# Kernel optimization log

Hardware: AMD Instinct MI355X
Metric: run time of the kernel (lower is better)

The kernel has to match this reference:

```python
import jax, jax.numpy as jnp
import numpy as np

# Graph/block sizes: 2-hop sampled minibatch
N0, N1, N2 = 655360, 81920, 8192   # src nodes layer0, dst0/src1, dst1 (seeds)
FAN0, FAN1 = 8, 10
E0, E1 = N1 * FAN0, N2 * FAN1       # 655360, 81920
F_IN, H = 128, 256
BN_EPS = 1e-5
L2_EPS = 1e-12


def setup_inputs() -> dict:
    key = jax.random.key(0)
    ks = jax.random.split(key, 16)
    s = 0.05  # param scale
    inp = {
        "x": jax.random.normal(ks[0], (N0, F_IN), jnp.float32),
        "edge_src0": jax.random.randint(ks[1], (E0,), 0, N0, jnp.int32),
        "edge_dst0": jnp.repeat(jnp.arange(N1, dtype=jnp.int32), FAN0),
        "edge_src1": jax.random.randint(ks[2], (E1,), 0, N1, jnp.int32),
        "edge_dst1": jnp.repeat(jnp.arange(N2, dtype=jnp.int32), FAN1),
        "W_pool0": jax.random.normal(ks[3], (F_IN, F_IN), jnp.float32) * s,
        "b_pool0": jnp.zeros((F_IN,), jnp.float32),
        "W_self0": jax.random.normal(ks[4], (F_IN, H), jnp.float32) * s,
        "W_neigh0": jax.random.normal(ks[5], (F_IN, H), jnp.float32) * s,
        "b0": jnp.zeros((H,), jnp.float32),
        "W_pool1": jax.random.normal(ks[6], (H, H), jnp.float32) * s,
        "b_pool1": jnp.zeros((H,), jnp.float32),
        "W_self1": jax.random.normal(ks[7], (H, H), jnp.float32) * s,
        "W_neigh1": jax.random.normal(ks[8], (H, H), jnp.float32) * s,
        "b1": jnp.zeros((H,), jnp.float32),
        "g_bn0": jnp.ones((H,), jnp.float32),
        "be_bn0": jnp.zeros((H,), jnp.float32),
        "W_h": jax.random.normal(ks[9], (H, H), jnp.float32) * s,
        "b_h": jnp.zeros((H,), jnp.float32),
        "g_bnh": jnp.ones((H,), jnp.float32),
        "be_bnh": jnp.zeros((H,), jnp.float32),
        "W_lat": jax.random.normal(ks[10], (H, H), jnp.float32) * s,
        "b_lat": jnp.zeros((H,), jnp.float32),
        "g_bnl": jnp.ones((H,), jnp.float32),
        "be_bnl": jnp.zeros((H,), jnp.float32),
    }
    return inp


def _sage_pool(h, esrc, edst, n_dst, Wp, bp, Ws, Wn, b):
    # DGL SAGEConv aggregator_type='pool':
    # m = relu(fc_pool(h_src)); pooled[v] = max_{u in N(v)} m[u]
    # out = fc_self(h_dst) + fc_neigh(pooled) + bias
    m = jax.nn.relu(h @ Wp + bp)                                  # [N_src, d]
    pooled = jax.ops.segment_max(m[esrc], edst, num_segments=n_dst)
    return h[:n_dst] @ Ws + pooled @ Wn + b


def _l2norm(h):
    n = jnp.sqrt(jnp.sum(h * h, axis=1, keepdims=True))
    return h / jnp.maximum(n, L2_EPS)


def _bn(h, g, b):
    mu = jnp.mean(h, axis=0)
    var = jnp.var(h, axis=0)
    return (h - mu) * jax.lax.rsqrt(var + BN_EPS) * g + b


def reference(x, edge_src0, edge_dst0, edge_src1, edge_dst1,
              W_pool0, b_pool0, W_self0, W_neigh0, b0,
              W_pool1, b_pool1, W_self1, W_neigh1, b1,
              g_bn0, be_bn0, W_h, b_h, g_bnh, be_bnh,
              W_lat, b_lat, g_bnl, be_bnl):
    # layer 0
    h = _sage_pool(x, edge_src0, edge_dst0, N1, W_pool0, b_pool0, W_self0, W_neigh0, b0)
    h = _l2norm(h)
    h = jax.nn.relu(_bn(h, g_bn0, be_bn0))
    # dropout: eval mode (identity)
    h = jax.nn.relu(_bn(h @ W_h + b_h, g_bnh, be_bnh))   # self.hidden
    # layer 1 (last conv)
    h = _sage_pool(h, edge_src1, edge_dst1, N2, W_pool1, b_pool1, W_self1, W_neigh1, b1)
    h = _l2norm(h)
    # self.latent
    h = _bn(h @ W_lat + b_lat, g_bnl, be_bnl)
    return h
```

## Files before the change

### kernel.cpp

```cpp
#include <hip/hip_runtime.h>

typedef unsigned short u16;
typedef unsigned int u32;
typedef float f32x4 __attribute__((ext_vector_type(4)));
typedef int i32x4 __attribute__((ext_vector_type(4)));
typedef __bf16 bf16x8 __attribute__((ext_vector_type(8)));
typedef short s16x8 __attribute__((ext_vector_type(8)));

#define CN0 655360
#define CN1 81920
#define CN2 8192

#define H0_OFF    0ull
#define T_OFF     41943040ull
#define H2_OFF    83886080ull
#define ZZ_OFF    88080384ull
#define WP0F_OFF  96468992ull
#define WC0F_OFF  96501760ull
#define WHF_OFF   96632832ull
#define WP1F_OFF  96763904ull
#define WC1F_OFF  96894976ull
#define WLATF_OFF 97157120ull
#define STAT_OFF  97288192ull
#define SS_OFF    97294336ull

__device__ inline u16 f2bf(float f) {
  u32 u = __builtin_bit_cast(u32, f);
  return (u16)((u + 0x7fffu + ((u >> 16) & 1u)) >> 16);
}
__device__ inline float bf2f(u16 s) {
  return __builtin_bit_cast(float, (u32)s << 16);
}

template <typename V>
__device__ inline auto mfma_sel(V a, V b, f32x4 c, int)
    -> decltype(__builtin_amdgcn_mfma_f32_16x16x32_bf16(a, b, c, 0, 0, 0)) {
  return __builtin_amdgcn_mfma_f32_16x16x32_bf16(a, b, c, 0, 0, 0);
}
template <typename V>
__device__ inline f32x4 mfma_sel(V a, V b, f32x4 c, long) {
  return __builtin_amdgcn_mfma_f32_16x16x32_bf16(
      __builtin_bit_cast(s16x8, a), __builtin_bit_cast(s16x8, b), c, 0, 0, 0);
}
__device__ inline f32x4 MFMA(i32x4 a, i32x4 b, f32x4 c) {
  return mfma_sel(__builtin_bit_cast(bf16x8, a), __builtin_bit_cast(bf16x8, b), c, 0);
}

__device__ void fragify(const float* W0, const float* W1, int Khalf, int N,
                        u16* dst, int tid, int nthr) {
  int K = W1 ? 2 * Khalf : Khalf;
  int ntile = N >> 4;
  int total = (K >> 5) * ntile * 512;
  for (int i = tid; i < total; i += nthr) {
    int j = i & 7;
    int lane = (i >> 3) & 63;
    int nt = (i >> 9) % ntile;
    int kt = i / (512 * ntile);
    int k = kt * 32 + ((lane >> 4) << 3) + j;
    int n = nt * 16 + (lane & 15);
    float v = (k < Khalf) ? W0[k * N + n] : W1[(k - Khalf) * N + n];
    dst[i] = f2bf(v);
  }
}

__global__ void kprep(const float* Wp0, const float* Ws0, const float* Wn0,
                      const float* Wh, const float* Wp1, const float* Ws1,
                      const float* Wn1, const float* Wlat,
                      u16* wp0f, u16* wc0f, u16* whf, u16* wp1f, u16* wc1f,
                      u16* wlatf) {
  int tid = blockIdx.x * blockDim.x + threadIdx.x;
  int nthr = gridDim.x * blockDim.x;
  fragify(Wp0, nullptr, 128, 128, wp0f, tid, nthr);
  fragify(Ws0, Wn0, 128, 256, wc0f, tid, nthr);
  fragify(Wh, nullptr, 256, 256, whf, tid, nthr);
  fragify(Wp1, nullptr, 256, 256, wp1f, tid, nthr);
  fragify(Ws1, Wn1, 256, 256, wc1f, tid, nthr);
  fragify(Wlat, nullptr, 256, 256, wlatf, tid, nthr);
}

__global__ void kfin(const float* __restrict__ stat, float inv_n,
                     const float* __restrict__ g, const float* __restrict__ be,
                     float* __restrict__ ssout) {
  int c = threadIdx.x;
  float mu = stat[c] * inv_n;
  float var = stat[256 + c] * inv_n - mu * mu;
  float sc = g[c] / sqrtf(var + 1e-5f);
  ssout[c] = sc;
  ssout[256 + c] = be[c] - mu * sc;
}

__global__ __launch_bounds__(256, 2)
void k1_layer0(const float* __restrict__ x, const int* __restrict__ esrc,
               const u16* __restrict__ wp0f, const u16* __restrict__ wc0f,
               const float* __restrict__ bp0, const float* __restrict__ b0v,
               u16* __restrict__ h0, float* __restrict__ stat0) {
  __shared__ __align__(16) char lds[81920];
  float* pooled = (float*)(lds + 65536);
  int tid = threadIdx.x, lane = tid & 63, w = tid >> 6;
  int r15 = lane & 15, g = lane >> 4;
  int d0 = blockIdx.x * 32;

  {
    int r = tid;
    int src = esrc[d0 * 8 + r];
    const float* xr = x + (size_t)src * 128;
    u32 rowb = (u32)r * 256, sw = (u32)((r & 7) << 4);
    for (int c = 0; c < 16; ++c) {
      f32x4 p0 = *(const f32x4*)(xr + c * 8);
      f32x4 p1 = *(const f32x4*)(xr + c * 8 + 4);
      union { i32x4 q; u16 h[8]; } pk;
      #pragma unroll
      for (int j = 0; j < 4; ++j) { pk.h[j] = f2bf(p0[j]); pk.h[4 + j] = f2bf(p1[j]); }
      *(i32x4*)(lds + ((rowb + (u32)c * 16) ^ sw)) = pk.q;
    }
  }
  __syncthreads();

  {
    i32x4 afr[4][4];
    #pragma unroll
    for (int rt = 0; rt < 4; ++rt)
      #pragma unroll
      for (int kt = 0; kt < 4; ++kt) {
        u32 r = (u32)(w * 64 + rt * 16 + r15);
        afr[rt][kt] = *(const i32x4*)(lds + ((r * 256 + (u32)kt * 64 + (u32)g * 16) ^ ((r & 7) << 4)));
      }
    for (int nt = 0; nt < 8; ++nt) {
      f32x4 acc[4] = {};
      #pragma unroll
      for (int kt = 0; kt < 4; ++kt) {
        i32x4 b = *(const i32x4*)(wp0f + (((kt * 8 + nt) * 64 + lane) << 3));
        #pragma unroll
        for (int rt = 0; rt < 4; ++rt) acc[rt] = MFMA(afr[rt][kt], b, acc[rt]);
      }
      float bias = bp0[nt * 16 + r15];
      #pragma unroll
      for (int rt = 0; rt < 4; ++rt) {
        float mx = fmaxf(fmaxf(acc[rt][0], acc[rt][1]), fmaxf(acc[rt][2], acc[rt][3]));
        mx = fmaxf(mx + bias, 0.0f);
        mx = fmaxf(mx, __shfl_xor(mx, 16));
        if ((g & 1) == 0)
          pooled[(w * 8 + rt * 2 + (g >> 1)) * 128 + nt * 16 + r15] = mx;
      }
    }
  }
  __syncthreads();

  float* h0buf = (float*)(lds + 16384);
  {
    int i = tid >> 3, seg = tid & 7;
    int k0 = seg * 32;
    u32 sw = (u32)((i & 7) << 4);
    float vals[32];
    if (seg < 4) {
      const float* xr = x + (size_t)(d0 + i) * 128 + k0;
      #pragma unroll
      for (int c4 = 0; c4 < 8; ++c4) {
        f32x4 t = *(const f32x4*)(xr + c4 * 4);
        vals[c4 * 4 + 0] = t[0]; vals[c4 * 4 + 1] = t[1];
        vals[c4 * 4 + 2] = t[2]; vals[c4 * 4 + 3] = t[3];
      }
    } else {
      const float* pr = pooled + i * 128 + (k0 - 128);
      #pragma unroll
      for (int c4 = 0; c4 < 8; ++c4) {
        f32x4 t = *(const f32x4*)(pr + c4 * 4);
        vals[c4 * 4 + 0] = t[0]; vals[c4 * 4 + 1] = t[1];
        vals[c4 * 4 + 2] = t[2]; vals[c4 * 4 + 3] = t[3];
      }
    }
    #pragma unroll
    for (int cc = 0; cc < 4; ++cc) {
      union { i32x4 q; u16 h[8]; } pk;
      #pragma unroll
      for (int j = 0; j < 8; ++j) pk.h[j] = f2bf(vals[cc * 8 + j]);
      *(i32x4*)(lds + (((u32)i * 512 + (u32)(k0 + cc * 8) * 2) ^ sw)) = pk.q;
    }
  }
  __syncthreads();

  {
    f32x4 acc[4][2] = {};
    for (int kt = 0; kt < 8; ++kt) {
      u32 r0 = (u32)r15, r1 = (u32)(16 + r15);
      i32x4 a0 = *(const i32x4*)(lds + ((r0 * 512 + (u32)kt * 64 + (u32)g * 16) ^ ((r0 & 7) << 4)));
      i32x4 a1 = *(const i32x4*)(lds + ((r1 * 512 + (u32)kt * 64 + (u32)g * 16) ^ ((r1 & 7) << 4)));
      #pragma unroll
      for (int n4 = 0; n4 < 4; ++n4) {
        int nt = w * 4 + n4;
        i32x4 b = *(const i32x4*)(wc0f + (((size_t)(kt * 16 + nt) * 64 + lane) << 3));
        acc[n4][0] = MFMA(a0, b, acc[n4][0]);
        acc[n4][1] = MFMA(a1, b, acc[n4][1]);
      }
    }
    #pragma unroll
    for (int n4 = 0; n4 < 4; ++n4) {
      int col = (w * 4 + n4) * 16 + r15;
      float bv = b0v[col];
      #pragma unroll
      for (int rt = 0; rt < 2; ++rt)
        #pragma unroll
        for (int j = 0; j < 4; ++j)
          h0buf[(rt * 16 + g * 4 + j) * 256 + col] = acc[n4][rt][j] + bv;
    }
  }
  __syncthreads();

  {
    int i = tid >> 3, part = tid & 7;
    float* hr = h0buf + i * 256 + part * 32;
    float v[32]; float ss = 0.0f;
    #pragma unroll
    for (int c = 0; c < 32; ++c) { v[c] = hr[c]; ss += v[c] * v[c]; }
    ss += __shfl_xor(ss, 1); ss += __shfl_xor(ss, 2); ss += __shfl_xor(ss, 4);
    float rn = 1.0f / fmaxf(sqrtf(ss), 1e-12f);
    u16* orow = h0 + (size_t)(d0 + i) * 256 + part * 32;
    #pragma unroll
    for (int cc = 0; cc < 4; ++cc) {
      union { i32x4 q; u16 h[8]; } pk;
      #pragma unroll
      for (int j = 0; j < 8; ++j) {
        float nv = v[cc * 8 + j] * rn;
        hr[cc * 8 + j] = nv;
        pk.h[j] = f2bf(nv);
      }
      *(i32x4*)(orow + cc * 8) = pk.q;
    }
  }
  __syncthreads();

  {
    int c = tid; float s1 = 0.0f, s2 = 0.0f;
    for (int r = 0; r < 32; ++r) { float vv = h0buf[r * 256 + c]; s1 += vv; s2 += vv * vv; }
    atomicAdd(&stat0[c], s1); atomicAdd(&stat0[256 + c], s2);
  }
}

template <bool RELU_OUT, bool STATS, bool H2OUT>
__global__ __launch_bounds__(256, 2)
void gemm64(const u16* __restrict__ Ain, const float* __restrict__ ss,
            const u16* __restrict__ Bf, const float* __restrict__ bias,
            u16* __restrict__ Out, float* __restrict__ stat,
            u16* __restrict__ H2out) {
  __shared__ __align__(16) char lds[67584];
  u16* tb = (u16*)(lds + 32768);
  float* scs = (float*)(lds + 65536);
  int tid = threadIdx.x, lane = tid & 63, w = tid >> 6;
  int r15 = lane & 15, g = lane >> 4;
  int d0 = blockIdx.x * 64;
  scs[tid] = ss[tid];
  scs[256 + tid] = ss[256 + tid];
  __syncthreads();

  {
    int i = tid >> 2, part = tid & 3;
    const u16* ar = Ain + (size_t)(d0 + i) * 256 + part * 64;
    u32 sw = (u32)((i & 7) << 4), rowb = (u32)i * 512;
    for (int cc = 0; cc < 8; ++cc) {
      union { i32x4 q; u16 h[8]; } in, out;
      in.q = *(const i32x4*)(ar + cc * 8);
      #pragma unroll
      for (int j = 0; j < 8; ++j) {
        int k = part * 64 + cc * 8 + j;
        float v = fmaxf(bf2f(in.h[j]) * scs[k] + scs[256 + k], 0.0f);
        out.h[j] = f2bf(v);
      }
      *(i32x4*)(lds + ((rowb + (u32)(part * 64 + cc * 8) * 2) ^ sw)) = out.q;
    }
  }
  __syncthreads();

  f32x4 acc[4][4] = {};
  for (int kt = 0; kt < 8; ++kt) {
    i32x4 a[4];
    #pragma unroll
    for (int rt = 0; rt < 4; ++rt) {
      u32 r = (u32)(rt * 16 + r15);
      a[rt] = *(const i32x4*)(lds + ((r * 512 + (u32)kt * 64 + (u32)g * 16) ^ ((r & 7) << 4)));
    }
    #pragma unroll
    for (int n4 = 0; n4 < 4; ++n4) {
      int nt = w * 4 + n4;
      i32x4 b = *(const i32x4*)(Bf + (((size_t)(kt * 16 + nt) * 64 + lane) << 3));
      #pragma unroll
      for (int rt = 0; rt < 4; ++rt) acc[n4][rt] = MFMA(a[rt], b, acc[n4][rt]);
    }
  }
  #pragma unroll
  for (int n4 = 0; n4 < 4; ++n4) {
    int col = (w * 4 + n4) * 16 + r15;
    float bv = bias[col];
    #pragma unroll
    for (int rt = 0; rt < 4; ++rt)
      #pragma unroll
      for (int j = 0; j < 4; ++j) {
        float v = acc[n4][rt][j] + bv;
        if (RELU_OUT) v = fmaxf(v, 0.0f);
        tb[(rt * 16 + g * 4 + j) * 256 + col] = f2bf(v);
      }
  }
  __syncthreads();

  {
    int i = tid >> 2, part = tid & 3;
    u16* orow = Out + (size_t)(d0 + i) * 256 + part * 64;
    const u16* trow = tb + i * 256 + part * 64;
    #pragma unroll
    for (int cc = 0; cc < 8; ++cc)
      *(i32x4*)(orow + cc * 8) = *(const i32x4*)(trow + cc * 8);
  }
  if (STATS) {
    int c = tid; float s1 = 0.0f, s2 = 0.0f;
    for (int r = 0; r < 64; ++r) { float v = bf2f(tb[r * 256 + c]); s1 += v; s2 += v * v; }
    atomicAdd(&stat[c], s1); atomicAdd(&stat[256 + c], s2);
  }
  if (H2OUT && d0 < CN2) {
    int i = tid >> 2, part = tid & 3;
    u16* orow = H2out + (size_t)(d0 + i) * 256 + part * 64;
    u32 sw = (u32)((i & 7) << 4);
    #pragma unroll
    for (int cc = 0; cc < 8; ++cc)
      *(i32x4*)(orow + cc * 8) =
          *(const i32x4*)(lds + (((u32)i * 512 + (u32)(part * 64 + cc * 8) * 2) ^ sw));
  }
}

__global__ __launch_bounds__(256, 2)
void k6_layer1(const int* __restrict__ esrc1, const u16* __restrict__ m1,
               const u16* __restrict__ h2, const u16* __restrict__ wc1f,
               const u16* __restrict__ wlatf, const float* __restrict__ b1v,
               const float* __restrict__ blat, float* __restrict__ zz,
               float* __restrict__ statl) {
  __shared__ __align__(16) char lds[81920];
  float* zbuf = (float*)(lds + 32768);
  int tid = threadIdx.x, lane = tid & 63, w = tid >> 6;
  int r15 = lane & 15, g = lane >> 4;
  int d0 = blockIdx.x * 32;

  {
    int i = tid >> 3, part = tid & 7;
    u32 sw = (u32)((i & 7) << 4);
    const u16* hrow = h2 + (size_t)(d0 + i) * 256 + part * 32;
    #pragma unroll
    for (int cc = 0; cc < 4; ++cc) {
      i32x4 q = *(const i32x4*)(hrow + cc * 8);
      *(i32x4*)(lds + (((u32)i * 1024 + (u32)(part * 32 + cc * 8) * 2) ^ sw)) = q;
    }
    float mx[32];
    #pragma unroll
    for (int c = 0; c < 32; ++c) mx[c] = -1e30f;
    for (int e = 0; e < 10; ++e) {
      int src = esrc1[(d0 + i) * 10 + e];
      const u16* mrow = m1 + (size_t)src * 256 + part * 32;
      #pragma unroll
      for (int cc = 0; cc < 4; ++cc) {
        union { i32x4 q; u16 h[8]; } pk;
        pk.q = *(const i32x4*)(mrow + cc * 8);
        #pragma unroll
        for (int j = 0; j < 8; ++j) mx[cc * 8 + j] = fmaxf(mx[cc * 8 + j], bf2f(pk.h[j]));
      }
    }
    #pragma unroll
    for (int cc = 0; cc < 4; ++cc) {
      union { i32x4 q; u16 h[8]; } pk;
      #pragma unroll
      for (int j = 0; j < 8; ++j) pk.h[j] = f2bf(mx[cc * 8 + j]);
      *(i32x4*)(lds + (((u32)i * 1024 + (u32)(256 + part * 32 + cc * 8) * 2) ^ sw)) = pk.q;
    }
  }
  __syncthreads();

  {
    f32x4 acc[4][2] = {};
    for (int kt = 0; kt < 16; ++kt) {
      u32 r0 = (u32)r15, r1 = (u32)(16 + r15);
      i32x4 a0 = *(const i32x4*)(lds + ((r0 * 1024 + (u32)kt * 64 + (u32)g * 16) ^ ((r0 & 7) << 4)));
      i32x4 a1 = *(const i32x4*)(lds + ((r1 * 1024 + (u32)kt * 64 + (u32)g * 16) ^ ((r1 & 7) << 4)));
      #pragma unroll
      for (int n4 = 0; n4 < 4; ++n4) {
        int nt = w * 4 + n4;
        i32x4 b = *(const i32x4*)(wc1f + (((size_t)(kt * 16 + nt) * 64 + lane) << 3));
        acc[n4][0] = MFMA(a0, b, acc[n4][0]);
        acc[n4][1] = MFMA(a1, b, acc[n4][1]);
      }
    }
    #pragma unroll
    for (int n4 = 0; n4 < 4; ++n4) {
      int col = (w * 4 + n4) * 16 + r15;
      float bv = b1v[col];
      #pragma unroll
      for (int rt = 0; rt < 2; ++rt)
        #pragma unroll
        for (int j = 0; j < 4; ++j)
          zbuf[(rt * 16 + g * 4 + j) * 256 + col] = acc[n4][rt][j] + bv;
    }
  }
  __syncthreads();

  {
    int i = tid >> 3, part = tid & 7;
    float* zr = zbuf + i * 256 + part * 32;
    float v[32]; float ss = 0.0f;
    #pragma unroll
    for (int c = 0; c < 32; ++c) { v[c] = zr[c]; ss += v[c] * v[c]; }
    ss += __shfl_xor(ss, 1); ss += __shfl_xor(ss, 2); ss += __shfl_xor(ss, 4);
    float rn = 1.0f / fmaxf(sqrtf(ss), 1e-12f);
    u32 sw = (u32)((i & 7) << 4);
    #pragma unroll
    for (int cc = 0; cc < 4; ++cc) {
      union { i32x4 q; u16 h[8]; } pk;
      #pragma unroll
      for (int j = 0; j < 8; ++j) pk.h[j] = f2bf(v[cc * 8 + j] * rn);
      *(i32x4*)(lds + 65536 + (((u32)i * 512 + (u32)(part * 32 + cc * 8) * 2) ^ sw)) = pk.q;
    }
  }
  __syncthreads();

  {
    f32x4 acc[4][2] = {};
    for (int kt = 0; kt < 8; ++kt) {
      u32 r0 = (u32)r15, r1 = (u32)(16 + r15);
      i32x4 a0 = *(const i32x4*)(lds + 65536 + ((r0 * 512 + (u32)kt * 64 + (u32)g * 16) ^ ((r0 & 7) << 4)));
      i32x4 a1 = *(const i32x4*)(lds + 65536 + ((r1 * 512 + (u32)kt * 64 + (u32)g * 16) ^ ((r1 & 7) << 4)));
      #pragma unroll
      for (int n4 = 0; n4 < 4; ++n4) {
        int nt = w * 4 + n4;
        i32x4 b = *(const i32x4*)(wlatf + (((size_t)(kt * 16 + nt) * 64 + lane) << 3));
        acc[n4][0] = MFMA(a0, b, acc[n4][0]);
        acc[n4][1] = MFMA(a1, b, acc[n4][1]);
      }
    }
    #pragma unroll
    for (int n4 = 0; n4 < 4; ++n4) {
      int col = (w * 4 + n4) * 16 + r15;
      float bv = blat[col];
      #pragma unroll
      for (int rt = 0; rt < 2; ++rt)
        #pragma unroll
        for (int j = 0; j < 4; ++j)
          zbuf[(rt * 16 + g * 4 + j) * 256 + col] = acc[n4][rt][j] + bv;
    }
  }
  __syncthreads();

  {
    int i = tid >> 3, part = tid & 7;
    float* zr = zbuf + i * 256 + part * 32;
    float* orow = zz + (size_t)(d0 + i) * 256 + part * 32;
    #pragma unroll
    for (int c = 0; c < 32; c += 4) *(f32x4*)(orow + c) = *(const f32x4*)(zr + c);
  }
  {
    int c = tid; float s1 = 0.0f, s2 = 0.0f;
    for (int r = 0; r < 32; ++r) { float v = zbuf[r * 256 + c]; s1 += v; s2 += v * v; }
    atomicAdd(&statl[c], s1); atomicAdd(&statl[256 + c], s2);
  }
}

__global__ void k7_out(const float* __restrict__ zz, const float* __restrict__ ssl,
                       float* __restrict__ out) {
  int idx = blockIdx.x * 256 + threadIdx.x;
  int e0 = idx * 4;
  int c = e0 & 255;
  f32x4 v = *(const f32x4*)(zz + e0);
  f32x4 sc = *(const f32x4*)(ssl + c);
  f32x4 sh = *(const f32x4*)(ssl + 256 + c);
  *(f32x4*)(out + e0) = v * sc + sh;
}

extern "C" void kernel_launch(void* const* d_in, const int* in_sizes, int n_in,
                              void* d_out, int out_size, void* d_ws, size_t ws_size,
                              hipStream_t stream) {
  const float* x     = (const float*)d_in[0];
  const int*   es0   = (const int*)d_in[1];
  const int*   es1   = (const int*)d_in[3];
  const float* Wp0   = (const float*)d_in[5];
  const float* bp0   = (const float*)d_in[6];
  const float* Ws0   = (const float*)d_in[7];
  const float* Wn0   = (const float*)d_in[8];
  const float* b0v   = (const float*)d_in[9];
  const float* Wp1   = (const float*)d_in[10];
  const float* bp1   = (const float*)d_in[11];
  const float* Ws1   = (const float*)d_in[12];
  const float* Wn1   = (const float*)d_in[13];
  const float* b1v   = (const float*)d_in[14];
  const float* gbn0  = (const float*)d_in[15];
  const float* bebn0 = (const float*)d_in[16];
  const float* Wh    = (const float*)d_in[17];
  const float* bh    = (const float*)d_in[18];
  const float* gbnh  = (const float*)d_in[19];
  const float* bebnh = (const float*)d_in[20];
  const float* Wlat  = (const float*)d_in[21];
  const float* blat  = (const float*)d_in[22];
  const float* gbnl  = (const float*)d_in[23];
  const float* bebnl = (const float*)d_in[24];

  char* ws = (char*)d_ws;
  u16* h0    = (u16*)(ws + H0_OFF);
  u16* tban  = (u16*)(ws + T_OFF);
  u16* m1    = (u16*)(ws + H0_OFF);
  u16* h2    = (u16*)(ws + H2_OFF);
  float* zz  = (float*)(ws + ZZ_OFF);
  u16* wp0f  = (u16*)(ws + WP0F_OFF);
  u16* wc0f  = (u16*)(ws + WC0F_OFF);
  u16* whf   = (u16*)(ws + WHF_OFF);
  u16* wp1f  = (u16*)(ws + WP1F_OFF);
  u16* wc1f  = (u16*)(ws + WC1F_OFF);
  u16* wlatf = (u16*)(ws + WLATF_OFF);
  float* stat = (float*)(ws + STAT_OFF);
  float* ssv  = (float*)(ws + SS_OFF);

  hipMemsetAsync(stat, 0, 6 * 256 * sizeof(float), stream);
  kprep<<<64, 256, 0, stream>>>(Wp0, Ws0, Wn0, Wh, Wp1, Ws1, Wn1, Wlat,
                                wp0f, wc0f, whf, wp1f, wc1f, wlatf);
  k1_layer0<<<CN1 / 32, 256, 0, stream>>>(x, es0, wp0f, wc0f, bp0, b0v, h0, stat);
  kfin<<<1, 256, 0, stream>>>(stat, 1.0f / CN1, gbn0, bebn0, ssv);
  gemm64<false, true, false><<<CN1 / 64, 256, 0, stream>>>(h0, ssv, whf, bh, tban,
                                                           stat + 512, nullptr);
  kfin<<<1, 256, 0, stream>>>(stat + 512, 1.0f / CN1, gbnh, bebnh, ssv + 512);
  gemm64<true, false, true><<<CN1 / 64, 256, 0, stream>>>(tban, ssv + 512, wp1f, bp1,
                                                          m1, nullptr, h2);
  k6_layer1<<<CN2 / 32, 256, 0, stream>>>(es1, m1, h2, wc1f, wlatf, b1v, blat, zz,
                                          stat + 1024);
  kfin<<<1, 256, 0, stream>>>(stat + 1024, 1.0f / CN2, gbnl, bebnl, ssv + 1024);
  k7_out<<<out_size / 1024, 256, 0, stream>>>(zz, ssv + 1024, (float*)d_out);
  (void)in_sizes; (void)n_in; (void)ws_size;
}
```

Before: 327.9 us.

## Shrink LDS in layer0 and gemm kernels, gather directly into MFMA fragments

The layer-0 kernel now loads gathered neighbor rows from global memory straight into MFMA A-fragments instead of staging them in LDS. It writes pooled results as bf16 into a 16.9KB buffer and does the L2 norm and BN statistics in registers with shuffles. The gemm64 kernel reuses the A-tile LDS region for the output tile, halving its LDS, and launch bounds rise to allow more blocks per CU. The aim is to raise occupancy and cut LDS traffic and barriers, at the cost of uncoalesced direct gathers and possible register pressure under the tighter launch bounds.

```diff
diff --git a/kernel.cpp b/kernel.cpp
--- a/kernel.cpp
+++ b/kernel.cpp
@@ -30,6 +30,12 @@
 }
 __device__ inline float bf2f(u16 s) {
   return __builtin_bit_cast(float, (u32)s << 16);
+}
+__device__ inline i32x4 cvt8(f32x4 a, f32x4 b) {
+  union { bf16x8 v; i32x4 q; } u;
+  #pragma unroll
+  for (int j = 0; j < 4; ++j) { u.v[j] = (__bf16)a[j]; u.v[4 + j] = (__bf16)b[j]; }
+  return u.q;
 }
 
 template <typename V>
@@ -89,41 +95,31 @@
   ssout[256 + c] = be[c] - mu * sc;
 }
 
-__global__ __launch_bounds__(256, 2)
+__global__ __launch_bounds__(256, 3)
 void k1_layer0(const float* __restrict__ x, const int* __restrict__ esrc,
                const u16* __restrict__ wp0f, const u16* __restrict__ wc0f,
                const float* __restrict__ bp0, const float* __restrict__ b0v,
                u16* __restrict__ h0, float* __restrict__ stat0) {
-  __shared__ __align__(16) char lds[81920];
-  float* pooled = (float*)(lds + 65536);
+  __shared__ __align__(16) char lds[16896];
+  float* rsb = (float*)(lds + 16384);
   int tid = threadIdx.x, lane = tid & 63, w = tid >> 6;
   int r15 = lane & 15, g = lane >> 4;
   int d0 = blockIdx.x * 32;
 
   {
-    int r = tid;
-    int src = esrc[d0 * 8 + r];
-    const float* xr = x + (size_t)src * 128;
-    u32 rowb = (u32)r * 256, sw = (u32)((r & 7) << 4);
-    for (int c = 0; c < 16; ++c) {
-      f32x4 p0 = *(const f32x4*)(xr + c * 8);
-      f32x4 p1 = *(const f32x4*)(xr + c * 8 + 4);
-      union { i32x4 q; u16 h[8]; } pk;
-      #pragma unroll
-      for (int j = 0; j < 4; ++j) { pk.h[j] = f2bf(p0[j]); pk.h[4 + j] = f2bf(p1[j]); }
-      *(i32x4*)(lds + ((rowb + (u32)c * 16) ^ sw)) = pk.q;
-    }
-  }
-  __syncthreads();
-
-  {
+    int e0 = d0 * 8 + w * 64;
+    const float* rp[4];
+    #pragma unroll
+    for (int rt = 0; rt < 4; ++rt)
+      rp[rt] = x + (size_t)esrc[e0 + rt * 16 + r15] * 128;
     i32x4 afr[4][4];
     #pragma unroll
     for (int rt = 0; rt < 4; ++rt)
       #pragma unroll
       for (int kt = 0; kt < 4; ++kt) {
-        u32 r = (u32)(w * 64 + rt * 16 + r15);
-        afr[rt][kt] = *(const i32x4*)(lds + ((r * 256 + (u32)kt * 64 + (u32)g * 16) ^ ((r & 7) << 4)));
+        f32x4 p0 = *(const f32x4*)(rp[rt] + kt * 32 + g * 8);
+        f32x4 p1 = *(const f32x4*)(rp[rt] + kt * 32 + g * 8 + 4);
+        afr[rt][kt] = cvt8(p0, p1);
       }
     for (int nt = 0; nt < 8; ++nt) {
       f32x4 acc[4] = {};
@@ -139,112 +135,116 @@
         float mx = fmaxf(fmaxf(acc[rt][0], acc[rt][1]), fmaxf(acc[rt][2], acc[rt][3]));
         mx = fmaxf(mx + bias, 0.0f);
         mx = fmaxf(mx, __shfl_xor(mx, 16));
-        if ((g & 1) == 0)
-          pooled[(w * 8 + rt * 2 + (g >> 1)) * 128 + nt * 16 + r15] = mx;
-      }
-    }
-  }
-  __syncthreads();
-
-  float* h0buf = (float*)(lds + 16384);
-  {
-    int i = tid >> 3, seg = tid & 7;
-    int k0 = seg * 32;
+        if ((g & 1) == 0) {
+          u32 row = (u32)(w * 8 + rt * 2 + (g >> 1));
+          u32 byte = (row * 512 + 256 + (u32)(nt * 16 + r15) * 2) ^ ((row & 7) << 4);
+          *(u16*)(lds + byte) = f2bf(mx);
+        }
+      }
+    }
+  }
+
+  {
+    int i = tid >> 3, part = tid & 7;
+    const float* xr = x + (size_t)(d0 + i) * 128 + part * 16;
+    f32x4 t0 = *(const f32x4*)(xr + 0);
+    f32x4 t1 = *(const f32x4*)(xr + 4);
+    f32x4 t2 = *(const f32x4*)(xr + 8);
+    f32x4 t3 = *(const f32x4*)(xr + 12);
     u32 sw = (u32)((i & 7) << 4);
-    float vals[32];
-    if (seg < 4) {
-      const float* xr = x + (size_t)(d0 + i) * 128 + k0;
-      #pragma unroll
-      for (int c4 = 0; c4 < 8; ++c4) {
-        f32x4 t = *(const f32x4*)(xr + c4 * 4);
-        vals[c4 * 4 + 0] = t[0]; vals[c4 * 4 + 1] = t[1];
-        vals[c4 * 4 + 2] = t[2]; vals[c4 * 4 + 3] = t[3];
-      }
-    } else {
-      const float* pr = pooled + i * 128 + (k0 - 128);
-      #pragma unroll
-      for (int c4 = 0; c4 < 8; ++c4) {
-        f32x4 t = *(const f32x4*)(pr + c4 * 4);
-        vals[c4 * 4 + 0] = t[0]; vals[c4 * 4 + 1] = t[1];
-        vals[c4 * 4 + 2] = t[2]; vals[c4 * 4 + 3] = t[3];
-      }
-    }
-    #pragma unroll
-    for (int cc = 0; cc < 4; ++cc) {
-      union { i32x4 q; u16 h[8]; } pk;
-      #pragma unroll
-      for (int j = 0; j < 8; ++j) pk.h[j] = f2bf(vals[cc * 8 + j]);
-      *(i32x4*)(lds + (((u32)i * 512 + (u32)(k0 + cc * 8) * 2) ^ sw)) = pk.q;
-    }
-  }
-  __syncthreads();
-
-  {
-    f32x4 acc[4][2] = {};
-    for (int kt = 0; kt < 8; ++kt) {
-      u32 r0 = (u32)r15, r1 = (u32)(16 + r15);
-      i32x4 a0 = *(const i32x4*)(lds + ((r0 * 512 + (u32)kt * 64 + (u32)g * 16) ^ ((r0 & 7) << 4)));
-      i32x4 a1 = *(const i32x4*)(lds + ((r1 * 512 + (u32)kt * 64 + (u32)g * 16) ^ ((r1 & 7) << 4)));
-      #pragma unroll
-      for (int n4 = 0; n4 < 4; ++n4) {
-        int nt = w * 4 + n4;
-        i32x4 b = *(const i32x4*)(wc0f + (((size_t)(kt * 16 + nt) * 64 + lane) << 3));
-        acc[n4][0] = MFMA(a0, b, acc[n4][0]);
-        acc[n4][1] = MFMA(a1, b, acc[n4][1]);
-      }
-    }
+    *(i32x4*)(lds + (((u32)i * 512 + (u32)part * 32) ^ sw)) = cvt8(t0, t1);
+    *(i32x4*)(lds + (((u32)i * 512 + (u32)part * 32 + 16) ^ sw)) = cvt8(t2, t3);
+  }
+  __syncthreads();
+
+  f32x4 acc2[4][2] = {};
+  for (int kt = 0; kt < 8; ++kt) {
+    u32 r0 = (u32)r15, r1 = (u32)(16 + r15);
+    i32x4 a0 = *(const i32x4*)(lds + ((r0 * 512 + (u32)kt * 64 + (u32)g * 16) ^ ((r0 & 7) << 4)));
+    i32x4 a1 = *(const i32x4*)(lds + ((r1 * 512 + (u32)kt * 64 + (u32)g * 16) ^ ((r1 & 7) << 4)));
     #pragma unroll
     for (int n4 = 0; n4 < 4; ++n4) {
-      int col = (w * 4 + n4) * 16 + r15;
-      float bv = b0v[col];
-      #pragma unroll
-      for (int rt = 0; rt < 2; ++rt)
-        #pragma unroll
-        for (int j = 0; j < 4; ++j)
-          h0buf[(rt * 16 + g * 4 + j) * 256 + col] = acc[n4][rt][j] + bv;
-    }
-  }
-  __syncthreads();
-
-  {
-    int i = tid >> 3, part = tid & 7;
-    float* hr = h0buf + i * 256 + part * 32;
-    float v[32]; float ss = 0.0f;
-    #pragma unroll
-    for (int c = 0; c < 32; ++c) { v[c] = hr[c]; ss += v[c] * v[c]; }
-    ss += __shfl_xor(ss, 1); ss += __shfl_xor(ss, 2); ss += __shfl_xor(ss, 4);
-    float rn = 1.0f / fmaxf(sqrtf(ss), 1e-12f);
-    u16* orow = h0 + (size_t)(d0 + i) * 256 + part * 32;
-    #pragma unroll
-    for (int cc = 0; cc < 4; ++cc) {
-      union { i32x4 q; u16 h[8]; } pk;
-      #pragma unroll
-      for (int j = 0; j < 8; ++j) {
-        float nv = v[cc * 8 + j] * rn;
-        hr[cc * 8 + j] = nv;
-        pk.h[j] = f2bf(nv);
-      }
-      *(i32x4*)(orow + cc * 8) = pk.q;
-    }
-  }
-  __syncthreads();
-
-  {
-    int c = tid; float s1 = 0.0f, s2 = 0.0f;
-    for (int r = 0; r < 32; ++r) { float vv = h0buf[r * 256 + c]; s1 += vv; s2 += vv * vv; }
-    atomicAdd(&stat0[c], s1); atomicAdd(&stat0[256 + c], s2);
+      int nt = w * 4 + n4;
+      i32x4 b = *(const i32x4*)(wc0f + (((size_t)(kt * 16 + nt) * 64 + lane) << 3));
+      acc2[n4][0] = MFMA(a0, b, acc2[n4][0]);
+      acc2[n4][1] = MFMA(a1, b, acc2[n4][1]);
+    }
+  }
+
+  float vn[4][2][4];
+  #pragma unroll
+  for (int n4 = 0; n4 < 4; ++n4) {
+    float bv = b0v[(w * 4 + n4) * 16 + r15];
+    #pragma unroll
+    for (int rt = 0; rt < 2; ++rt)
+      #pragma unroll
+      for (int j = 0; j < 4; ++j) vn[n4][rt][j] = acc2[n4][rt][j] + bv;
+  }
+  float ssq[2][4];
+  #pragma unroll
+  for (int rt = 0; rt < 2; ++rt)
+    #pragma unroll
+    for (int j = 0; j < 4; ++j) {
+      float s = 0.0f;
+      #pragma unroll
+      for (int n4 = 0; n4 < 4; ++n4) s += vn[n4][rt][j] * vn[n4][rt][j];
+      s += __shfl_xor(s, 1); s += __shfl_xor(s, 2);
+      s += __shfl_xor(s, 4); s += __shfl_xor(s, 8);
+      ssq[rt][j] = s;
+      if (r15 == 0) rsb[(rt * 16 + g * 4 + j) * 4 + w] = s;
+    }
+  __syncthreads();
+
+  #pragma unroll
+  for (int rt = 0; rt < 2; ++rt)
+    #pragma unroll
+    for (int j = 0; j < 4; ++j) {
+      int r = rt * 16 + g * 4 + j;
+      f32x4 q = *(const f32x4*)&rsb[r * 4];
+      float rn = 1.0f / fmaxf(sqrtf(q[0] + q[1] + q[2] + q[3]), 1e-12f);
+      #pragma unroll
+      for (int n4 = 0; n4 < 4; ++n4) vn[n4][rt][j] *= rn;
+    }
+  #pragma unroll
+  for (int n4 = 0; n4 < 4; ++n4) {
+    int col = (w * 4 + n4) * 16 + r15;
+    float s1 = 0.0f, s2 = 0.0f;
+    #pragma unroll
+    for (int rt = 0; rt < 2; ++rt)
+      #pragma unroll
+      for (int j = 0; j < 4; ++j) { float v = vn[n4][rt][j]; s1 += v; s2 += v * v; }
+    s1 += __shfl_xor(s1, 16); s1 += __shfl_xor(s1, 32);
+    s2 += __shfl_xor(s2, 16); s2 += __shfl_xor(s2, 32);
+    if (g == 0) { atomicAdd(&stat0[col], s1); atomicAdd(&stat0[256 + col], s2); }
+  }
+  #pragma unroll
+  for (int n4 = 0; n4 < 4; ++n4)
+    #pragma unroll
+    for (int rt = 0; rt < 2; ++rt)
+      #pragma unroll
+      for (int j = 0; j < 4; ++j)
+        *(u16*)(lds + (u32)(rt * 16 + g * 4 + j) * 512 + (u32)((w * 4 + n4) * 16 + r15) * 2)
+            = f2bf(vn[n4][rt][j]);
+  __syncthreads();
+  {
+    int i = tid >> 3, c8 = tid & 7;
+    const char* srcp = lds + i * 512 + c8 * 64;
+    u16* dst = h0 + (size_t)(d0 + i) * 256 + c8 * 32;
+    #pragma unroll
+    for (int c = 0; c < 4; ++c)
+      *(i32x4*)(dst + c * 8) = *(const i32x4*)(srcp + c * 16);
   }
 }
 
 template <bool RELU_OUT, bool STATS, bool H2OUT>
-__global__ __launch_bounds__(256, 2)
+__global__ __launch_bounds__(256, 4)
 void gemm64(const u16* __restrict__ Ain, const float* __restrict__ ss,
             const u16* __restrict__ Bf, const float* __restrict__ bias,
             u16* __restrict__ Out, float* __restrict__ stat,
             u16* __restrict__ H2out) {
-  __shared__ __align__(16) char lds[67584];
-  u16* tb = (u16*)(lds + 32768);
-  float* scs = (float*)(lds + 65536);
+  __shared__ __align__(16) char lds[34816];
+  u16* tb = (u16*)lds;
+  float* scs = (float*)(lds + 32768);
   int tid = threadIdx.x, lane = tid & 63, w = tid >> 6;
   int r15 = lane & 15, g = lane >> 4;
   int d0 = blockIdx.x * 64;
@@ -286,6 +286,21 @@
       for (int rt = 0; rt < 4; ++rt) acc[n4][rt] = MFMA(a[rt], b, acc[n4][rt]);
     }
   }
+  __syncthreads();
+
+  if constexpr (H2OUT) {
+    if (d0 < CN2) {
+      int i = tid >> 2, part = tid & 3;
+      u16* orow = H2out + (size_t)(d0 + i) * 256 + part * 64;
+      u32 sw = (u32)((i & 7) << 4);
+      #pragma unroll
+      for (int cc = 0; cc < 8; ++cc)
+        *(i32x4*)(orow + cc * 8) =
+            *(const i32x4*)(lds + (((u32)i * 512 + (u32)(part * 64 + cc * 8) * 2) ^ sw));
+    }
+    __syncthreads();
+  }
+
   #pragma unroll
   for (int n4 = 0; n4 < 4; ++n4) {
     int col = (w * 4 + n4) * 16 + r15;
@@ -313,15 +328,6 @@
     int c = tid; float s1 = 0.0f, s2 = 0.0f;
     for (int r = 0; r < 64; ++r) { float v = bf2f(tb[r * 256 + c]); s1 += v; s2 += v * v; }
     atomicAdd(&stat[c], s1); atomicAdd(&stat[256 + c], s2);
-  }
-  if (H2OUT && d0 < CN2) {
-    int i = tid >> 2, part = tid & 3;
-    u16* orow = H2out + (size_t)(d0 + i) * 256 + part * 64;
-    u32 sw = (u32)((i & 7) << 4);
-    #pragma unroll
-    for (int cc = 0; cc < 8; ++cc)
-      *(i32x4*)(orow + cc * 8) =
-          *(const i32x4*)(lds + (((u32)i * 512 + (u32)(part * 64 + cc * 8) * 2) ^ sw));
   }
 }
 
```

Result: faster. 283.4 us (-13.6%).
